# Kernel tuning notes

Measured on AMD Instinct MI355X. Metric: run time of the kernel, lower is better.

## Reference

```python
import jax, jax.numpy as jnp
import numpy as np

NODE = 480      # 3 groups x 160 per-node MLPs
H = 20          # network_unit
B = 16384       # T_N time points


def setup_inputs() -> dict:
    key = jax.random.key(0)
    ks = jax.random.split(key, 9)
    s1 = 1.0            # Linear(1,H): kaiming-uniform-ish bound ~ 1/sqrt(1)
    sh = 1.0 / np.sqrt(H)
    return {
        "inputs": jax.random.normal(ks[0], (B, NODE), dtype=jnp.float32),
        # one stacked weight set for all 480 independent tiny MLPs
        "W1": jax.random.uniform(ks[1], (NODE, H), jnp.float32, -s1, s1),
        "b1": jax.random.uniform(ks[2], (NODE, H), jnp.float32, -s1, s1),
        "W2": jax.random.uniform(ks[3], (NODE, H, H), jnp.float32, -sh, sh),
        "b2": jax.random.uniform(ks[4], (NODE, H), jnp.float32, -sh, sh),
        "W3": jax.random.uniform(ks[5], (NODE, H, H), jnp.float32, -sh, sh),
        "b3": jax.random.uniform(ks[6], (NODE, H), jnp.float32, -sh, sh),
        "W4": jax.random.uniform(ks[7], (NODE, H), jnp.float32, -sh, sh),
        "b4": jax.random.uniform(ks[8], (NODE,), jnp.float32, -sh, sh),
    }


def reference(inputs, W1, b1, W2, b2, W3, b3, W4, b4):
    # Each of the 480 columns of `inputs` feeds its own 1->20->20->20->1 tanh MLP.
    # Batched over the node axis g instead of a Python loop over 480 blocks.
    x = inputs                                    # [B, G]
    h = jnp.tanh(x[:, :, None] * W1 + b1)          # [B, G, H]  (Linear(1,H))
    h = jnp.tanh(jnp.einsum('bgk,gkl->bgl', h, W2) + b2)   # [B, G, H]
    h = jnp.tanh(jnp.einsum('bgk,gkl->bgl', h, W3) + b3)   # [B, G, H]
    out = jnp.einsum('bgk,gk->bg', h, W4) + b4     # [B, G]  (Linear(H,1))
    return out
```

## Files before the change

### kernel.cpp

```cpp
#include <hip/hip_runtime.h>

#define H 20
#define NODE 480
#define BATCH 16384
#define BLK 256

typedef float v2f __attribute__((ext_vector_type(2)));

__device__ __forceinline__ float fast_tanh(float x) {
    float t = __builtin_amdgcn_exp2f(x * 2.8853900817779268f);
    return 1.0f - 2.0f * __builtin_amdgcn_rcpf(t + 1.0f);
}
__device__ __forceinline__ v2f tanh2(v2f v) {
    v2f r; r.x = fast_tanh(v.x); r.y = fast_tanh(v.y); return r;
}

__global__ __launch_bounds__(256) void transpose_in(const float* __restrict__ src,
                                                    float* __restrict__ dst) {
    __shared__ float t[32][33];
    const int gT = blockIdx.x * 32, bT = blockIdx.y * 32;
    const int tx = threadIdx.x, ty = threadIdx.y;
#pragma unroll
    for (int j = 0; j < 32; j += 8)
        t[ty + j][tx] = src[(bT + ty + j) * NODE + gT + tx];
    __syncthreads();
#pragma unroll
    for (int j = 0; j < 32; j += 8)
        dst[(gT + ty + j) * BATCH + bT + tx] = t[tx][ty + j];
}

__global__ __launch_bounds__(256) void transpose_out(const float* __restrict__ src,
                                                     float* __restrict__ dst) {
    __shared__ float t[32][33];
    const int gT = blockIdx.x * 32, bT = blockIdx.y * 32;
    const int tx = threadIdx.x, ty = threadIdx.y;
#pragma unroll
    for (int j = 0; j < 32; j += 8)
        t[ty + j][tx] = src[(gT + ty + j) * BATCH + bT + tx];
    __syncthreads();
#pragma unroll
    for (int j = 0; j < 32; j += 8)
        dst[(bT + ty + j) * NODE + gT + tx] = t[tx][ty + j];
}

template <bool TR>
__global__ __launch_bounds__(BLK, 1) void mlp480_kernel(
    const float* __restrict__ inputs,
    const float* __restrict__ W1, const float* __restrict__ b1,
    const float* __restrict__ W2, const float* __restrict__ b2,
    const float* __restrict__ W3, const float* __restrict__ b3,
    const float* __restrict__ W4, const float* __restrict__ b4,
    float* __restrict__ out)
{
    const int g = blockIdx.x;
    const int b = blockIdx.y * BLK + threadIdx.x;

    const v2f* __restrict__ w1v = (const v2f*)(W1 + g * H);
    const v2f* __restrict__ b1v = (const v2f*)(b1 + g * H);
    const v2f* __restrict__ b2v = (const v2f*)(b2 + g * H);
    const v2f* __restrict__ b3v = (const v2f*)(b3 + g * H);
    const v2f* __restrict__ w4v = (const v2f*)(W4 + g * H);
    const float* __restrict__ w2 = W2 + g * H * H;
    const float* __restrict__ w3 = W3 + g * H * H;
    const float bias4 = b4[g];

    const float x = TR ? inputs[g * BATCH + b] : inputs[b * NODE + g];
    const v2f x2 = {x, x};

    v2f h2[10], a2[10];

#pragma unroll
    for (int j = 0; j < 10; ++j)
        h2[j] = tanh2(x2 * w1v[j] + b1v[j]);

#pragma unroll
    for (int l = 0; l < 10; ++l) a2[l] = b2v[l];
#pragma unroll
    for (int k = 0; k < H; ++k) {
        const float hk = (k & 1) ? h2[k >> 1].y : h2[k >> 1].x;
        const v2f hk2 = {hk, hk};
        const v2f* __restrict__ row = (const v2f*)(w2 + k * H);
#pragma unroll
        for (int l = 0; l < 10; ++l) a2[l] = hk2 * row[l] + a2[l];
    }
#pragma unroll
    for (int l = 0; l < 10; ++l) h2[l] = tanh2(a2[l]);

#pragma unroll
    for (int l = 0; l < 10; ++l) a2[l] = b3v[l];
#pragma unroll
    for (int k = 0; k < H; ++k) {
        const float hk = (k & 1) ? h2[k >> 1].y : h2[k >> 1].x;
        const v2f hk2 = {hk, hk};
        const v2f* __restrict__ row = (const v2f*)(w3 + k * H);
#pragma unroll
        for (int l = 0; l < 10; ++l) a2[l] = hk2 * row[l] + a2[l];
    }
#pragma unroll
    for (int l = 0; l < 10; ++l) h2[l] = tanh2(a2[l]);

    v2f s2 = {bias4, 0.0f};
#pragma unroll
    for (int k = 0; k < 10; ++k) s2 = h2[k] * w4v[k] + s2;
    const float o = s2.x + s2.y;

    if (TR) out[g * BATCH + b] = o;
    else    out[b * NODE + g] = o;
}

extern "C" void kernel_launch(void* const* d_in, const int* in_sizes, int n_in,
                              void* d_out, int out_size, void* d_ws, size_t ws_size,
                              hipStream_t stream) {
    const float* inputs = (const float*)d_in[0];
    const float* W1 = (const float*)d_in[1];
    const float* b1 = (const float*)d_in[2];
    const float* W2 = (const float*)d_in[3];
    const float* b2 = (const float*)d_in[4];
    const float* W3 = (const float*)d_in[5];
    const float* b3 = (const float*)d_in[6];
    const float* W4 = (const float*)d_in[7];
    const float* b4 = (const float*)d_in[8];
    float* out = (float*)d_out;

    const size_t planeBytes = (size_t)BATCH * NODE * sizeof(float);
    const dim3 mlpGrid(NODE, BATCH / BLK);

    if (ws_size >= 2 * planeBytes) {
        float* in_t  = (float*)d_ws;
        float* out_t = (float*)((char*)d_ws + planeBytes);
        dim3 tGrid(NODE / 32, BATCH / 32), tBlk(32, 8);
        transpose_in<<<tGrid, tBlk, 0, stream>>>(inputs, in_t);
        mlp480_kernel<true><<<mlpGrid, BLK, 0, stream>>>(in_t, W1, b1, W2, b2,
                                                         W3, b3, W4, b4, out_t);
        transpose_out<<<tGrid, tBlk, 0, stream>>>(out_t, out);
    } else {
        mlp480_kernel<false><<<mlpGrid, BLK, 0, stream>>>(inputs, W1, b1, W2, b2,
                                                          W3, b3, W4, b4, out);
    }
}
```

Baseline: 288.7 us.

## Fuse transposes into MLP kernel by processing four nodes per thread with vector I/O

Removes the separate input and output transpose kernels and their workspace round trips. Each thread now handles four adjacent nodes for one batch row, loading and storing them as a single 16-byte vector directly in the original row-major layout. Occupancy hints change from launch_bounds(256,1) to waves_per_eu(1,5). The per-thread work quadruples, which may raise register pressure, and the row-strided vector accesses are less coalesced than the transposed layout.

New measurement: 306.3 us. +6.1%, slower.

```diff
diff --git a/kernel.cpp b/kernel.cpp
--- a/kernel.cpp
+++ b/kernel.cpp
@@ -4,8 +4,10 @@
 #define NODE 480
 #define BATCH 16384
 #define BLK 256
+#define GPT 4
 
 typedef float v2f __attribute__((ext_vector_type(2)));
+typedef float v4f __attribute__((ext_vector_type(4)));
 
 __device__ __forceinline__ float fast_tanh(float x) {
     float t = __builtin_amdgcn_exp2f(x * 2.8853900817779268f);
@@ -15,36 +17,9 @@
     v2f r; r.x = fast_tanh(v.x); r.y = fast_tanh(v.y); return r;
 }
 
-__global__ __launch_bounds__(256) void transpose_in(const float* __restrict__ src,
-                                                    float* __restrict__ dst) {
-    __shared__ float t[32][33];
-    const int gT = blockIdx.x * 32, bT = blockIdx.y * 32;
-    const int tx = threadIdx.x, ty = threadIdx.y;
-#pragma unroll
-    for (int j = 0; j < 32; j += 8)
-        t[ty + j][tx] = src[(bT + ty + j) * NODE + gT + tx];
-    __syncthreads();
-#pragma unroll
-    for (int j = 0; j < 32; j += 8)
-        dst[(gT + ty + j) * BATCH + bT + tx] = t[tx][ty + j];
-}
-
-__global__ __launch_bounds__(256) void transpose_out(const float* __restrict__ src,
-                                                     float* __restrict__ dst) {
-    __shared__ float t[32][33];
-    const int gT = blockIdx.x * 32, bT = blockIdx.y * 32;
-    const int tx = threadIdx.x, ty = threadIdx.y;
-#pragma unroll
-    for (int j = 0; j < 32; j += 8)
-        t[ty + j][tx] = src[(gT + ty + j) * BATCH + bT + tx];
-    __syncthreads();
-#pragma unroll
-    for (int j = 0; j < 32; j += 8)
-        dst[(bT + ty + j) * NODE + gT + tx] = t[tx][ty + j];
-}
-
-template <bool TR>
-__global__ __launch_bounds__(BLK, 1) void mlp480_kernel(
+__global__ __attribute__((amdgpu_flat_work_group_size(BLK, BLK),
+                          amdgpu_waves_per_eu(1, 5)))
+void mlp480_fused(
     const float* __restrict__ inputs,
     const float* __restrict__ W1, const float* __restrict__ b1,
     const float* __restrict__ W2, const float* __restrict__ b2,
@@ -52,60 +27,70 @@
     const float* __restrict__ W4, const float* __restrict__ b4,
     float* __restrict__ out)
 {
-    const int g = blockIdx.x;
-    const int b = blockIdx.y * BLK + threadIdx.x;
+    const int g0 = blockIdx.x * GPT;
+    const int b  = blockIdx.y * BLK + threadIdx.x;
+    const size_t rowoff = (size_t)b * NODE + g0;
 
-    const v2f* __restrict__ w1v = (const v2f*)(W1 + g * H);
-    const v2f* __restrict__ b1v = (const v2f*)(b1 + g * H);
-    const v2f* __restrict__ b2v = (const v2f*)(b2 + g * H);
-    const v2f* __restrict__ b3v = (const v2f*)(b3 + g * H);
-    const v2f* __restrict__ w4v = (const v2f*)(W4 + g * H);
-    const float* __restrict__ w2 = W2 + g * H * H;
-    const float* __restrict__ w3 = W3 + g * H * H;
-    const float bias4 = b4[g];
-
-    const float x = TR ? inputs[g * BATCH + b] : inputs[b * NODE + g];
-    const v2f x2 = {x, x};
-
-    v2f h2[10], a2[10];
+    const v4f xv = *(const v4f*)(inputs + rowoff);
+    const float xs[GPT] = {xv.x, xv.y, xv.z, xv.w};
+    float os[GPT];
 
 #pragma unroll
-    for (int j = 0; j < 10; ++j)
-        h2[j] = tanh2(x2 * w1v[j] + b1v[j]);
+    for (int gi = 0; gi < GPT; ++gi) {
+        const int g = g0 + gi;
+
+        const v2f* __restrict__ w1v = (const v2f*)(W1 + g * H);
+        const v2f* __restrict__ b1v = (const v2f*)(b1 + g * H);
+        const v2f* __restrict__ b2v = (const v2f*)(b2 + g * H);
+        const v2f* __restrict__ b3v = (const v2f*)(b3 + g * H);
+        const v2f* __restrict__ w4v = (const v2f*)(W4 + g * H);
+        const float* __restrict__ w2 = W2 + g * H * H;
+        const float* __restrict__ w3 = W3 + g * H * H;
+        const float bias4 = b4[g];
+
+        const float x = xs[gi];
+        const v2f x2 = {x, x};
+
+        v2f h2[10], a2[10];
 
 #pragma unroll
-    for (int l = 0; l < 10; ++l) a2[l] = b2v[l];
-#pragma unroll
-    for (int k = 0; k < H; ++k) {
-        const float hk = (k & 1) ? h2[k >> 1].y : h2[k >> 1].x;
-        const v2f hk2 = {hk, hk};
-        const v2f* __restrict__ row = (const v2f*)(w2 + k * H);
-#pragma unroll
-        for (int l = 0; l < 10; ++l) a2[l] = hk2 * row[l] + a2[l];
-    }
-#pragma unroll
-    for (int l = 0; l < 10; ++l) h2[l] = tanh2(a2[l]);
+        for (int j = 0; j < 10; ++j)
+            h2[j] = tanh2(x2 * w1v[j] + b1v[j]);
 
 #pragma unroll
-    for (int l = 0; l < 10; ++l) a2[l] = b3v[l];
+        for (int l = 0; l < 10; ++l) a2[l] = b2v[l];
 #pragma unroll
-    for (int k = 0; k < H; ++k) {
-        const float hk = (k & 1) ? h2[k >> 1].y : h2[k >> 1].x;
-        const v2f hk2 = {hk, hk};
-        const v2f* __restrict__ row = (const v2f*)(w3 + k * H);
+        for (int k = 0; k < H; ++k) {
+            const float hk = (k & 1) ? h2[k >> 1].y : h2[k >> 1].x;
+            const v2f hk2 = {hk, hk};
+            const v2f* __restrict__ row = (const v2f*)(w2 + k * H);
 #pragma unroll
-        for (int l = 0; l < 10; ++l) a2[l] = hk2 * row[l] + a2[l];
+            for (int l = 0; l < 10; ++l) a2[l] = hk2 * row[l] + a2[l];
+        }
+#pragma unroll
+        for (int l = 0; l < 10; ++l) h2[l] = tanh2(a2[l]);
+
+#pragma unroll
+        for (int l = 0; l < 10; ++l) a2[l] = b3v[l];
+#pragma unroll
+        for (int k = 0; k < H; ++k) {
+            const float hk = (k & 1) ? h2[k >> 1].y : h2[k >> 1].x;
+            const v2f hk2 = {hk, hk};
+            const v2f* __restrict__ row = (const v2f*)(w3 + k * H);
+#pragma unroll
+            for (int l = 0; l < 10; ++l) a2[l] = hk2 * row[l] + a2[l];
+        }
+#pragma unroll
+        for (int l = 0; l < 10; ++l) h2[l] = tanh2(a2[l]);
+
+        v2f s2 = {bias4, 0.0f};
+#pragma unroll
+        for (int k = 0; k < 10; ++k) s2 = h2[k] * w4v[k] + s2;
+        os[gi] = s2.x + s2.y;
     }
-#pragma unroll
-    for (int l = 0; l < 10; ++l) h2[l] = tanh2(a2[l]);
 
-    v2f s2 = {bias4, 0.0f};
-#pragma unroll
-    for (int k = 0; k < 10; ++k) s2 = h2[k] * w4v[k] + s2;
-    const float o = s2.x + s2.y;
-
-    if (TR) out[g * BATCH + b] = o;
-    else    out[b * NODE + g] = o;
+    v4f ov = {os[0], os[1], os[2], os[3]};
+    *(v4f*)(out + rowoff) = ov;
 }
 
 extern "C" void kernel_launch(void* const* d_in, const int* in_sizes, int n_in,
@@ -122,19 +107,7 @@
     const float* b4 = (const float*)d_in[8];
     float* out = (float*)d_out;
 
-    const size_t planeBytes = (size_t)BATCH * NODE * sizeof(float);
-    const dim3 mlpGrid(NODE, BATCH / BLK);
-
-    if (ws_size >= 2 * planeBytes) {
-        float* in_t  = (float*)d_ws;
-        float* out_t = (float*)((char*)d_ws + planeBytes);
-        dim3 tGrid(NODE / 32, BATCH / 32), tBlk(32, 8);
-        transpose_in<<<tGrid, tBlk, 0, stream>>>(inputs, in_t);
-        mlp480_kernel<true><<<mlpGrid, BLK, 0, stream>>>(in_t, W1, b1, W2, b2,
-                                                         W3, b3, W4, b4, out_t);
-        transpose_out<<<tGrid, tBlk, 0, stream>>>(out_t, out);
-    } else {
-        mlp480_kernel<false><<<mlpGrid, BLK, 0, stream>>>(inputs, W1, b1, W2, b2,
-                                                          W3, b3, W4, b4, out);
-    }
+    dim3 grid(NODE / GPT, BATCH / BLK);
+    mlp480_fused<<<grid, BLK, 0, stream>>>(inputs, W1, b1, W2, b2,
+                                           W3, b3, W4, b4, out);
 }
```
